# Kernel tuning notes

Hardware: AMD Instinct MI355X
Metric: run time of the kernel (lower is better)

## Reference

```python
import jax, jax.numpy as jnp
import numpy as np

B, N, D, P = 16, 128, 1024, 128  # batch, seq_len, n_in, n_mlp
SCALE = 0  # scores divided by P**SCALE (supar convention); scale=0 => no-op


def setup_inputs() -> dict:
    key = jax.random.key(0)
    ks = jax.random.split(key, 6)
    s_in = 1.0 / np.sqrt(D)   # keep MLP activations ~unit scale
    s_w = 1.0 / P             # keep triple-product scores bounded
    return {
        "x": jax.random.normal(ks[0], (B, N, D), jnp.float32),
        "x_span": jax.random.normal(ks[1], (B, N, D), jnp.float32),
        # MLP projections (Linear weight stored torch-style as (out, in))
        "Wx": jax.random.normal(ks[2], (P, D), jnp.float32) * s_in,
        "bx": jnp.zeros((P,), jnp.float32),
        "Wy": jax.random.normal(ks[3], (P, D), jnp.float32) * s_in,
        "by": jnp.zeros((P,), jnp.float32),
        "Wz": jax.random.normal(ks[4], (P, D), jnp.float32) * s_in,
        "bz": jnp.zeros((P,), jnp.float32),
        # Triaffine weight: (P+1 [bias_x], P [z, no bias], P+1 [bias_y]), n_out=1 squeezed
        "W3": jax.random.normal(ks[5], (P + 1, P, P + 1), jnp.float32) * s_w,
    }


def _mlp(h, W, b):
    # supar MLP: Linear + LeakyReLU(0.1); dropout=0 at inference
    return jax.nn.leaky_relu(h @ W.T + b, 0.1)


def reference(x, x_span, Wx, bx, Wy, by, Wz, bz, W3):
    xp = _mlp(x_span, Wx, bx)  # (B,N,P)  -> triaffine arg x
    yp = _mlp(x_span, Wy, by)  # (B,N,P)  -> triaffine arg y
    zp = _mlp(x, Wz, bz)       # (B,N,P)  -> triaffine arg z (head words)
    ones = jnp.ones((B, N, 1), xp.dtype)
    x1 = jnp.concatenate([xp, ones], axis=-1)  # bias_x
    y1 = jnp.concatenate([yp, ones], axis=-1)  # bias_y
    # w: per-head-word bilinear map, (B,N,P+1,P+1)
    w = jnp.einsum('bzk,ikj->bzij', zp, W3)
    # s: (B, z, x, y) = (B,N,N,N)
    s = jnp.einsum('bxi,bzij,byj->bzxy', x1, w, y1)
    s = s / (P ** SCALE)
    # Span2oScorer: s.permute(0, 2, 3, 1).float() -> (B, span_i, span_j, head)
    return jnp.transpose(s, (0, 2, 3, 1)).astype(jnp.float32)
```

## Files before the change

### kernel.cpp

```cpp
#include <hip/hip_runtime.h>

typedef __bf16 bf16;
typedef __bf16 bf16x8 __attribute__((ext_vector_type(8)));
typedef __bf16 bf16x4 __attribute__((ext_vector_type(4)));
typedef float f32x4 __attribute__((ext_vector_type(4)));

#define MFMA(a, b, c) __builtin_amdgcn_mfma_f32_16x16x32_bf16((a), (b), (c), 0, 0, 0)

static __device__ __forceinline__ f32x4 zero4() {
    f32x4 z; z[0] = 0.f; z[1] = 0.f; z[2] = 0.f; z[3] = 0.f; return z;
}

__global__ __launch_bounds__(256) void k_prep(
    const float* __restrict__ x, const float* __restrict__ xsp,
    const float* __restrict__ Wx, const float* __restrict__ Wy, const float* __restrict__ Wz,
    const float* __restrict__ W3,
    bf16* __restrict__ xb, bf16* __restrict__ xspb, bf16* __restrict__ wbf,
    bf16* __restrict__ w3b, float* __restrict__ w3bias)
{
    const int b = blockIdx.x, t = threadIdx.x;
    if (b < 1120) {
        const float* src; bf16* dst; int base;
        if (b < 512)       { src = xsp; dst = xspb; base = b * 4096; }
        else if (b < 1024) { src = x;   dst = xb;   base = (b - 512) * 4096; }
        else {
            int i = b - 1024;
            int proj = i >> 5;
            src = (proj == 0) ? Wx : (proj == 1) ? Wy : Wz;
            dst = wbf + proj * 131072;
            base = (i & 31) * 4096;
        }
        int o = base + t * 16;
#pragma unroll
        for (int u = 0; u < 4; u++) {
            float4 v = *(const float4*)(src + o + u * 4);
            bf16x4 w; w[0] = (bf16)v.x; w[1] = (bf16)v.y; w[2] = (bf16)v.z; w[3] = (bf16)v.w;
            *(bf16x4*)(dst + o + u * 4) = w;
        }
    } else {
        int nb = b - 1120;
        int n = nb * 8 + (t >> 5);
        int c = t & 31;
        const float* row = W3 + n * 129;
        bf16x4 w;
        w[0] = (bf16)row[4 * c + 0];
        w[1] = (bf16)row[4 * c + 1];
        w[2] = (bf16)row[4 * c + 2];
        w[3] = (bf16)row[4 * c + 3];
        *(bf16x4*)(w3b + n * 136 + 4 * c) = w;
        if (c == 0) w3bias[n] = row[128];
    }
}

__global__ __launch_bounds__(256) void k_mlp(
    const bf16* __restrict__ xspb, const bf16* __restrict__ xb,
    const bf16* __restrict__ wbf,
    const float* __restrict__ bx, const float* __restrict__ by, const float* __restrict__ bz,
    bf16* __restrict__ pout)
{
    const int proj = blockIdx.y;
    const bf16* A = (proj == 2) ? xb : xspb;
    const bf16* W = wbf + proj * 131072;
    const float* bias = (proj == 0) ? bx : (proj == 1) ? by : bz;
    bf16* out = pout + proj * 262144;

    const int tid = threadIdx.x;
    const int wv = tid >> 6, lane = tid & 63, quad = lane >> 4, lr = lane & 15;
    const int m0 = blockIdx.x * 64 + wv * 16;

    f32x4 acc[8];
#pragma unroll
    for (int i = 0; i < 8; i++) acc[i] = zero4();

    const bf16* brow = A + (m0 + lr) * 1024 + quad * 8;
    const bf16* arow = W + lr * 1024 + quad * 8;

    for (int kw = 0; kw < 32; kw++) {
        bf16x8 bfr = *(const bf16x8*)(brow + kw * 32);
#pragma unroll
        for (int pt = 0; pt < 8; pt++) {
            bf16x8 af = *(const bf16x8*)(arow + pt * 16 * 1024 + kw * 32);
            acc[pt] = MFMA(af, bfr, acc[pt]);
        }
    }
#pragma unroll
    for (int pt = 0; pt < 8; pt++) {
        int p = pt * 16 + quad * 4;
        float4 bv = *(const float4*)(bias + p);
        int m = m0 + lr;
        bf16x4 o;
        float v0 = acc[pt][0] + bv.x; o[0] = (bf16)(v0 > 0.f ? v0 : 0.1f * v0);
        float v1 = acc[pt][1] + bv.y; o[1] = (bf16)(v1 > 0.f ? v1 : 0.1f * v1);
        float v2 = acc[pt][2] + bv.z; o[2] = (bf16)(v2 > 0.f ? v2 : 0.1f * v2);
        float v3 = acc[pt][3] + bv.w; o[3] = (bf16)(v3 > 0.f ? v3 : 0.1f * v3);
        *(bf16x4*)(out + m * 128 + p) = o;
    }
}

__global__ __launch_bounds__(256) void k_vgemm(
    const bf16* __restrict__ yp,
    const bf16* __restrict__ w3b,
    const float* __restrict__ w3bias,
    bf16* __restrict__ V)
{
    __shared__ bf16 Vt[128 * 136];
    const int b = blockIdx.y;
    const int n0 = blockIdx.x * 128;
    const int tid = threadIdx.x;
    const int wv = tid >> 6, lane = tid & 63, quad = lane >> 4, lr = lane & 15;
    const int y0 = wv * 32;

    const bf16* Ab = yp + b * 16384;

    f32x4 acc[8][2];
#pragma unroll
    for (int nt = 0; nt < 8; nt++) { acc[nt][0] = zero4(); acc[nt][1] = zero4(); }

#pragma unroll
    for (int kw = 0; kw < 4; kw++) {
        bf16x8 b0 = *(const bf16x8*)(Ab + (y0 + lr) * 128 + kw * 32 + quad * 8);
        bf16x8 b1 = *(const bf16x8*)(Ab + (y0 + 16 + lr) * 128 + kw * 32 + quad * 8);
#pragma unroll
        for (int nt = 0; nt < 8; nt++) {
            bf16x8 af = *(const bf16x8*)(w3b + (n0 + nt * 16 + lr) * 136 + kw * 32 + quad * 8);
            acc[nt][0] = MFMA(af, b0, acc[nt][0]);
            acc[nt][1] = MFMA(af, b1, acc[nt][1]);
        }
    }
#pragma unroll
    for (int nt = 0; nt < 8; nt++) {
        int nl = nt * 16 + quad * 4;
        float4 bv = *(const float4*)(w3bias + n0 + nl);
#pragma unroll
        for (int s = 0; s < 2; s++) {
            int y = y0 + s * 16 + lr;
            bf16x4 o;
            o[0] = (bf16)(acc[nt][s][0] + bv.x);
            o[1] = (bf16)(acc[nt][s][1] + bv.y);
            o[2] = (bf16)(acc[nt][s][2] + bv.z);
            o[3] = (bf16)(acc[nt][s][3] + bv.w);
            *(bf16x4*)(&Vt[y * 136 + nl]) = o;
        }
    }
    __syncthreads();
    const int yr = tid >> 4, nn = (tid & 15) * 8;
#pragma unroll
    for (int pass = 0; pass < 8; pass++) {
        int y = pass * 16 + yr;
        bf16x8 v = *(const bf16x8*)(&Vt[y * 136 + nn]);
        *(bf16x8*)(V + (b * 128 + y) * 16512 + n0 + nn) = v;
    }
}

__global__ __launch_bounds__(512) void k_score(
    const bf16* __restrict__ xp,
    const bf16* __restrict__ zp,
    const bf16* __restrict__ V,
    float* __restrict__ out)
{
    __shared__ __align__(16) bf16 Vl[129 * 136];
    __shared__ float Hb[128];
    const int bi = blockIdx.x;
    const int b = bi >> 7, y = bi & 127;
    const int tid = threadIdx.x;
    const int wv = tid >> 6, lane = tid & 63, quad = lane >> 4, lr = lane & 15;
    const int r0 = wv * 16 + lr;

    const bf16* Zb = zp + b * 16384;
    const bf16* Xb = xp + b * 16384;
    const bf16* Vby = V + (b * 128 + y) * 16512;

    bf16x8 bz[4], bx[4];
#pragma unroll
    for (int kw = 0; kw < 4; kw++) bz[kw] = *(const bf16x8*)(Zb + r0 * 128 + kw * 32 + quad * 8);
#pragma unroll
    for (int iw = 0; iw < 4; iw++) bx[iw] = *(const bf16x8*)(Xb + r0 * 128 + iw * 32 + quad * 8);

    for (int c = tid; c < 2064; c += 512) {
        bf16x8 v = *(const bf16x8*)(Vby + c * 8);
        *(bf16x8*)(&Vl[(c >> 4) * 136 + (c & 15) * 8]) = v;
    }
    __syncthreads();

    f32x4 acc1[9];
#pragma unroll
    for (int it = 0; it < 9; it++) acc1[it] = zero4();

#pragma unroll
    for (int kw = 0; kw < 4; kw++) {
#pragma unroll
        for (int it = 0; it < 8; it++) {
            bf16x8 af = *(const bf16x8*)(&Vl[(it * 16 + lr) * 136 + kw * 32 + quad * 8]);
            acc1[it] = MFMA(af, bz[kw], acc1[it]);
        }
        bf16x8 a8;
#pragma unroll
        for (int q = 0; q < 8; q++) a8[q] = (bf16)0.f;
        if (lr == 0) a8 = *(const bf16x8*)(&Vl[128 * 136 + kw * 32 + quad * 8]);
        acc1[8] = MFMA(a8, bz[kw], acc1[8]);
    }
    __syncthreads();

#pragma unroll
    for (int it = 0; it < 8; it++) {
        int i = it * 16 + quad * 4;
        bf16x4 o;
        o[0] = (bf16)acc1[it][0];
        o[1] = (bf16)acc1[it][1];
        o[2] = (bf16)acc1[it][2];
        o[3] = (bf16)acc1[it][3];
        *(bf16x4*)(&Vl[r0 * 136 + i]) = o;
    }
    if (quad == 0) Hb[r0] = acc1[8][0];
    __syncthreads();

    f32x4 acc2[8];
#pragma unroll
    for (int zt = 0; zt < 8; zt++) acc2[zt] = zero4();

#pragma unroll
    for (int iw = 0; iw < 4; iw++) {
#pragma unroll
        for (int zt = 0; zt < 8; zt++) {
            bf16x8 ah = *(const bf16x8*)(&Vl[(zt * 16 + lr) * 136 + iw * 32 + quad * 8]);
            acc2[zt] = MFMA(ah, bx[iw], acc2[zt]);
        }
    }
#pragma unroll
    for (int zt = 0; zt < 8; zt++) {
        int zb = zt * 16 + quad * 4;
        f32x4 hb = *(const f32x4*)(&Hb[zb]);
        int xx = r0;
        f32x4 o;
        o[0] = acc2[zt][0] + hb[0];
        o[1] = acc2[zt][1] + hb[1];
        o[2] = acc2[zt][2] + hb[2];
        o[3] = acc2[zt][3] + hb[3];
        *(f32x4*)(out + (((b * 128 + xx) * 128 + y) * 128 + zb)) = o;
    }
}

extern "C" void kernel_launch(void* const* d_in, const int* in_sizes, int n_in,
                              void* d_out, int out_size, void* d_ws, size_t ws_size,
                              hipStream_t stream) {
    const float* x   = (const float*)d_in[0];
    const float* xsp = (const float*)d_in[1];
    const float* Wx  = (const float*)d_in[2];
    const float* bx  = (const float*)d_in[3];
    const float* Wy  = (const float*)d_in[4];
    const float* by  = (const float*)d_in[5];
    const float* Wz  = (const float*)d_in[6];
    const float* bz  = (const float*)d_in[7];
    const float* W3  = (const float*)d_in[8];
    float* out = (float*)d_out;

    char* ws = (char*)d_ws;
    bf16*  xspb   = (bf16*)(ws);
    bf16*  xb     = (bf16*)(ws + 4194304);
    bf16*  wbf    = (bf16*)(ws + 8388608);
    bf16*  w3b    = (bf16*)(ws + 9175040);
    bf16*  pout   = (bf16*)(ws + 13666304);
    bf16*  V      = (bf16*)(ws + 15239168);
    float* w3bias = (float*)(ws + 82872320);

    k_prep<<<3184, 256, 0, stream>>>(x, xsp, Wx, Wy, Wz, W3, xb, xspb, wbf, w3b, w3bias);
    k_mlp<<<dim3(32, 3), 256, 0, stream>>>(xspb, xb, wbf, bx, by, bz, pout);
    k_vgemm<<<dim3(129, 16), 256, 0, stream>>>(pout + 262144 , w3b, w3bias, V);
    k_score<<<2048, 512, 0, stream>>>(pout , pout + 524288 , V, out);
}
```

Before: 296.4 us.

## Spread MLP GEMM over more blocks and batch V staging loads in score kernel

The MLP projection kernel now gives each block 16 rows, with the four waves splitting the 128 output columns between them. This raises the grid from 96 to 384 blocks so more of the GPU is busy, at the cost of re-reading the activation rows in every wave. In the score kernel, all global loads of the V slice are issued up front into registers before being written to shared memory, and the x-fragment loads are deferred until after the first GEMM to cut register pressure. Occupancy hints are also added to launch_bounds for the vgemm and score kernels.

```diff
diff --git a/kernel.cpp b/kernel.cpp
--- a/kernel.cpp
+++ b/kernel.cpp
@@ -66,38 +66,37 @@
 
     const int tid = threadIdx.x;
     const int wv = tid >> 6, lane = tid & 63, quad = lane >> 4, lr = lane & 15;
-    const int m0 = blockIdx.x * 64 + wv * 16;
-
-    f32x4 acc[8];
-#pragma unroll
-    for (int i = 0; i < 8; i++) acc[i] = zero4();
+    const int m0 = blockIdx.x * 16;
+
+    f32x4 acc[2];
+    acc[0] = zero4(); acc[1] = zero4();
 
     const bf16* brow = A + (m0 + lr) * 1024 + quad * 8;
-    const bf16* arow = W + lr * 1024 + quad * 8;
-
+    const bf16* arow = W + (wv * 16 + lr) * 1024 + quad * 8;
+
+#pragma unroll 4
     for (int kw = 0; kw < 32; kw++) {
         bf16x8 bfr = *(const bf16x8*)(brow + kw * 32);
-#pragma unroll
-        for (int pt = 0; pt < 8; pt++) {
-            bf16x8 af = *(const bf16x8*)(arow + pt * 16 * 1024 + kw * 32);
-            acc[pt] = MFMA(af, bfr, acc[pt]);
-        }
-    }
-#pragma unroll
-    for (int pt = 0; pt < 8; pt++) {
-        int p = pt * 16 + quad * 4;
+        bf16x8 a0 = *(const bf16x8*)(arow + kw * 32);
+        bf16x8 a1 = *(const bf16x8*)(arow + 65536 + kw * 32);
+        acc[0] = MFMA(a0, bfr, acc[0]);
+        acc[1] = MFMA(a1, bfr, acc[1]);
+    }
+#pragma unroll
+    for (int s = 0; s < 2; s++) {
+        int p = (wv + s * 4) * 16 + quad * 4;
         float4 bv = *(const float4*)(bias + p);
         int m = m0 + lr;
         bf16x4 o;
-        float v0 = acc[pt][0] + bv.x; o[0] = (bf16)(v0 > 0.f ? v0 : 0.1f * v0);
-        float v1 = acc[pt][1] + bv.y; o[1] = (bf16)(v1 > 0.f ? v1 : 0.1f * v1);
-        float v2 = acc[pt][2] + bv.z; o[2] = (bf16)(v2 > 0.f ? v2 : 0.1f * v2);
-        float v3 = acc[pt][3] + bv.w; o[3] = (bf16)(v3 > 0.f ? v3 : 0.1f * v3);
+        float v0 = acc[s][0] + bv.x; o[0] = (bf16)(v0 > 0.f ? v0 : 0.1f * v0);
+        float v1 = acc[s][1] + bv.y; o[1] = (bf16)(v1 > 0.f ? v1 : 0.1f * v1);
+        float v2 = acc[s][2] + bv.z; o[2] = (bf16)(v2 > 0.f ? v2 : 0.1f * v2);
+        float v3 = acc[s][3] + bv.w; o[3] = (bf16)(v3 > 0.f ? v3 : 0.1f * v3);
         *(bf16x4*)(out + m * 128 + p) = o;
     }
 }
 
-__global__ __launch_bounds__(256) void k_vgemm(
+__global__ __launch_bounds__(256, 4) void k_vgemm(
     const bf16* __restrict__ yp,
     const bf16* __restrict__ w3b,
     const float* __restrict__ w3bias,
@@ -152,7 +151,7 @@
     }
 }
 
-__global__ __launch_bounds__(512) void k_score(
+__global__ __launch_bounds__(512, 4) void k_score(
     const bf16* __restrict__ xp,
     const bf16* __restrict__ zp,
     const bf16* __restrict__ V,
@@ -170,16 +169,24 @@
     const bf16* Xb = xp + b * 16384;
     const bf16* Vby = V + (b * 128 + y) * 16512;
 
-    bf16x8 bz[4], bx[4];
+    bf16x8 st[4];
+#pragma unroll
+    for (int u = 0; u < 4; u++) st[u] = *(const bf16x8*)(Vby + (tid + u * 512) * 8);
+    bf16x8 st4;
+#pragma unroll
+    for (int q = 0; q < 8; q++) st4[q] = (bf16)0.f;
+    if (tid < 16) st4 = *(const bf16x8*)(Vby + (2048 + tid) * 8);
+
+    bf16x8 bz[4];
 #pragma unroll
     for (int kw = 0; kw < 4; kw++) bz[kw] = *(const bf16x8*)(Zb + r0 * 128 + kw * 32 + quad * 8);
-#pragma unroll
-    for (int iw = 0; iw < 4; iw++) bx[iw] = *(const bf16x8*)(Xb + r0 * 128 + iw * 32 + quad * 8);
-
-    for (int c = tid; c < 2064; c += 512) {
-        bf16x8 v = *(const bf16x8*)(Vby + c * 8);
-        *(bf16x8*)(&Vl[(c >> 4) * 136 + (c & 15) * 8]) = v;
-    }
+
+#pragma unroll
+    for (int u = 0; u < 4; u++) {
+        int c = tid + u * 512;
+        *(bf16x8*)(&Vl[(c >> 4) * 136 + (c & 15) * 8]) = st[u];
+    }
+    if (tid < 16) *(bf16x8*)(&Vl[128 * 136 + tid * 8]) = st4;
     __syncthreads();
 
     f32x4 acc1[9];
@@ -200,6 +207,10 @@
         acc1[8] = MFMA(a8, bz[kw], acc1[8]);
     }
     __syncthreads();
+
+    bf16x8 bxf[4];
+#pragma unroll
+    for (int iw = 0; iw < 4; iw++) bxf[iw] = *(const bf16x8*)(Xb + r0 * 128 + iw * 32 + quad * 8);
 
 #pragma unroll
     for (int it = 0; it < 8; it++) {
@@ -223,7 +234,7 @@
 #pragma unroll
         for (int zt = 0; zt < 8; zt++) {
             bf16x8 ah = *(const bf16x8*)(&Vl[(zt * 16 + lr) * 136 + iw * 32 + quad * 8]);
-            acc2[zt] = MFMA(ah, bx[iw], acc2[zt]);
+            acc2[zt] = MFMA(ah, bxf[iw], acc2[zt]);
         }
     }
 #pragma unroll
@@ -264,7 +275,7 @@
     float* w3bias = (float*)(ws + 82872320);
 
     k_prep<<<3184, 256, 0, stream>>>(x, xsp, Wx, Wy, Wz, W3, xb, xspb, wbf, w3b, w3bias);
-    k_mlp<<<dim3(32, 3), 256, 0, stream>>>(xspb, xb, wbf, bx, by, bz, pout);
+    k_mlp<<<dim3(128, 3), 256, 0, stream>>>(xspb, xb, wbf, bx, by, bz, pout);
     k_vgemm<<<dim3(129, 16), 256, 0, stream>>>(pout + 262144 , w3b, w3bias, V);
     k_score<<<2048, 512, 0, stream>>>(pout , pout + 524288 , V, out);
 }
```

New measurement: 251.6 us. 15.1% less time.
